# Performance work log

Hardware: AMD Instinct MI355X
Metric: run time of the kernel (lower is better)

The kernel has to match this reference:

```python
import jax, jax.numpy as jnp
import numpy as np

N_NODES = 100000
N_EDGES = 1600000
IN_FEATS = 128
N_HIDDEN = 128
OUT_DIM = 32
BN_EPS = 1e-5


def setup_inputs() -> dict:
    key = jax.random.key(0)
    ks = jax.random.split(key, 12)
    s = 0.05  # weight init scale
    return {
        "features": jax.random.normal(ks[0], (N_NODES, IN_FEATS), dtype=jnp.float32),
        "src": jax.random.randint(ks[1], (N_EDGES,), 0, N_NODES),
        "dst": jax.random.randint(ks[2], (N_EDGES,), 0, N_NODES),
        # layer 0: in_feats -> n_hidden
        "Ws0": jax.random.normal(ks[3], (IN_FEATS, N_HIDDEN), dtype=jnp.float32) * s,
        "Wn0": jax.random.normal(ks[4], (IN_FEATS, N_HIDDEN), dtype=jnp.float32) * s,
        "b0": jnp.zeros((N_HIDDEN,), jnp.float32),
        # layer 1: n_hidden -> n_hidden
        "Ws1": jax.random.normal(ks[5], (N_HIDDEN, N_HIDDEN), dtype=jnp.float32) * s,
        "Wn1": jax.random.normal(ks[6], (N_HIDDEN, N_HIDDEN), dtype=jnp.float32) * s,
        "b1": jnp.zeros((N_HIDDEN,), jnp.float32),
        # layer 2 (output): n_hidden -> out_dim, no activation
        "Ws2": jax.random.normal(ks[7], (N_HIDDEN, OUT_DIM), dtype=jnp.float32) * s,
        "Wn2": jax.random.normal(ks[8], (N_HIDDEN, OUT_DIM), dtype=jnp.float32) * s,
        "b2": jnp.zeros((OUT_DIM,), jnp.float32),
        # batch norms after layers 0 and 1
        "g0": jnp.ones((N_HIDDEN,), jnp.float32),
        "be0": jnp.zeros((N_HIDDEN,), jnp.float32),
        "g1": jnp.ones((N_HIDDEN,), jnp.float32),
        "be1": jnp.zeros((N_HIDDEN,), jnp.float32),
    }


def _sage_mean(h, src, dst, inv_deg, Ws, Wn, b):
    # DGL SAGEConv('mean'): fc_self(h) + fc_neigh(mean of in-neighbor feats)
    agg = jax.ops.segment_sum(h[src], dst, num_segments=N_NODES) * inv_deg
    return h @ Ws + agg @ Wn + b


def _batch_norm(h, gamma, beta):
    mu = jnp.mean(h, axis=0)
    var = jnp.var(h, axis=0)
    return (h - mu) * jax.lax.rsqrt(var + BN_EPS) * gamma + beta


def reference(features, src, dst, Ws0, Wn0, b0, Ws1, Wn1, b1, Ws2, Wn2, b2, g0, be0, g1, be1):
    ones = jnp.ones((N_EDGES,), jnp.float32)
    deg = jax.ops.segment_sum(ones, dst, num_segments=N_NODES)
    inv_deg = (1.0 / jnp.maximum(deg, 1.0))[:, None]  # [N,1]

    # layer 0: SAGEConv internal activation, then BN + external activation
    h = jax.nn.relu(_sage_mean(features, src, dst, inv_deg, Ws0, Wn0, b0))
    h = jax.nn.relu(_batch_norm(h, g0, be0))
    # layer 1 (hidden)
    h = jax.nn.relu(_sage_mean(h, src, dst, inv_deg, Ws1, Wn1, b1))
    h = jax.nn.relu(_batch_norm(h, g1, be1))
    # layer 2 (output): no activation, no BN (idx > n_hidden_layers)
    h = _sage_mean(h, src, dst, inv_deg, Ws2, Wn2, b2)

    # dgl.mean_nodes over a single graph -> [1, out_dim], then softmax over classes
    hg = jnp.mean(h, axis=0, keepdims=True)
    return jax.nn.softmax(hg, axis=1)
```

## Files before the change

kernel.cpp:

```cpp
#include <hip/hip_runtime.h>
#include <hip/hip_bf16.h>

typedef __hip_bfloat16 bf16;
typedef __hip_bfloat162 bf162;

#define NN 100000
#define NE 1600000
#define BN_EPS 1e-5f

#define BSH 8
#define NBUCK ((NN + 255) >> BSH)
#define ABLK 128
#define EPBA ((NE + ABLK - 1) / ABLK)
#define CAP 6144
#define CAPP 5120

struct alignas(16) bf16x8 { bf16 v[8]; };

typedef __bf16 bfrag __attribute__((ext_vector_type(8)));
typedef float f4 __attribute__((ext_vector_type(4)));
typedef float f16v __attribute__((ext_vector_type(16)));
typedef float f2 __attribute__((ext_vector_type(2)));

static __device__ __forceinline__ float b2f(bf16 x){ return __bfloat162float(x); }
static __device__ __forceinline__ bf16 f2b(float x){ return __float2bfloat16(x); }

static __device__ __forceinline__ uint2 pk8_fp8(float x0,float x1,float x2,float x3,
                                                float x4,float x5,float x6,float x7)
{
    int lo = __builtin_amdgcn_cvt_pk_fp8_f32(x0, x1, 0, 0);
    lo = __builtin_amdgcn_cvt_pk_fp8_f32(x2, x3, lo, 1);
    int hi = __builtin_amdgcn_cvt_pk_fp8_f32(x4, x5, 0, 0);
    hi = __builtin_amdgcn_cvt_pk_fp8_f32(x6, x7, hi, 1);
    return make_uint2((unsigned)lo, (unsigned)hi);
}

__global__ __launch_bounds__(256) void k_convert(const float* __restrict__ in,
                                                 unsigned char* __restrict__ outf8, int n)
{
    int i = (blockIdx.x * 256 + threadIdx.x) * 8;
    if (i + 7 < n) {
        float4 a = *(const float4*)(in + i);
        float4 b = *(const float4*)(in + i + 4);
        *(uint2*)(outf8 + i) = pk8_fp8(a.x,a.y,a.z,a.w,b.x,b.y,b.z,b.w);
    }
}

__global__ __launch_bounds__(256) void k_wtrans(const float* __restrict__ W0, const float* __restrict__ W1,
                                                const float* __restrict__ W2, const float* __restrict__ W3,
                                                bf16* __restrict__ T0, bf16* __restrict__ T1,
                                                bf16* __restrict__ T2, bf16* __restrict__ T3)
{
    int m = blockIdx.x >> 6;
    int t = (blockIdx.x & 63) * 256 + threadIdx.x;
    const float* W = (m == 0) ? W0 : (m == 1) ? W1 : (m == 2) ? W2 : W3;
    bf16* T = (m == 0) ? T0 : (m == 1) ? T1 : (m == 2) ? T2 : T3;
    int j = t & 7;
    int lane = (t >> 3) & 63;
    int frag = t >> 9;
    int ks = frag >> 2, ct = frag & 3;
    int k = ks * 16 + (lane >> 5) * 8 + j;
    int n = ct * 32 + (lane & 31);
    T[t] = f2b(W[k * 128 + n]);
}

__global__ __launch_bounds__(256) void k_pa12(const int* __restrict__ src, const int* __restrict__ dst,
                                              int* __restrict__ gcurD, int* __restrict__ gcurS,
                                              unsigned* __restrict__ packD, unsigned* __restrict__ packS)
{
    __shared__ int histD[NBUCK], histS[NBUCK];
    __shared__ int baseD[NBUCK], baseS[NBUCK];
    __shared__ int curD[NBUCK],  curS[NBUCK];
    int t = threadIdx.x;
    for (int i = t; i < NBUCK; i += 256) { histD[i] = 0; histS[i] = 0; curD[i] = 0; curS[i] = 0; }
    __syncthreads();
    int e0 = blockIdx.x * EPBA, e1 = min(e0 + EPBA, NE);
    for (int e = e0 + t; e < e1; e += 256) {
        unsigned bd = ((unsigned)dst[e]) >> BSH;
        unsigned bs = ((unsigned)src[e]) >> BSH;
        if (bd < (unsigned)NBUCK) atomicAdd(&histD[bd], 1);
        if (bs < (unsigned)NBUCK) atomicAdd(&histS[bs], 1);
    }
    __syncthreads();
    for (int i = t; i < NBUCK; i += 256) {
        baseD[i] = (histD[i] > 0) ? atomicAdd(&gcurD[i], histD[i]) : 0;
        baseS[i] = (histS[i] > 0) ? atomicAdd(&gcurS[i], histS[i]) : 0;
    }
    __syncthreads();
    for (int e = e0 + t; e < e1; e += 256) {
        int s = src[e], d = dst[e];
        unsigned bd = ((unsigned)d) >> BSH;
        if (bd < (unsigned)NBUCK) {
            int r = baseD[bd] + atomicAdd(&curD[bd], 1);
            if (r < CAPP)
                packD[(size_t)bd * CAPP + r] = (((unsigned)d & 255u) << 24) | ((unsigned)s & 0xFFFFFFu);
        }
        unsigned bs = ((unsigned)s) >> BSH;
        if (bs < (unsigned)NBUCK) {
            int r = baseS[bs] + atomicAdd(&curS[bs], 1);
            if (r < CAPP)
                packS[(size_t)bs * CAPP + r] = (((unsigned)s & 255u) << 24) | ((unsigned)d & 0xFFFFFFu);
        }
    }
}

__global__ __launch_bounds__(512) void k_bscan(const int* __restrict__ cnt, int* __restrict__ start)
{
    __shared__ int sd[512];
    int t = threadIdx.x;
    int v = (t < NBUCK) ? cnt[t] : 0;
    sd[t] = v;
    __syncthreads();
    for (int o = 1; o < 512; o <<= 1) {
        int x = (t >= o) ? sd[t - o] : 0;
        __syncthreads();
        sd[t] += x;
        __syncthreads();
    }
    if (t < NBUCK) start[t] = sd[t] - v;
    if (t == 0) start[NBUCK] = NE;
}

__global__ __launch_bounds__(256) void k_pbD(const unsigned* __restrict__ packD, const int* __restrict__ bucketStartD,
                                             int* __restrict__ offs, float* __restrict__ invd,
                                             int* __restrict__ esrc)
{
    __shared__ int dcnt[256];
    __shared__ int sscan[256];
    __shared__ int cur[256];
    __shared__ int S[CAP];
    int t = threadIdx.x;
    int b = blockIdx.x;
    int base = b << BSH;
    dcnt[t] = 0;
    cur[t] = 0;
    for (int i = t; i < CAP; i += 256) S[i] = 0;
    __syncthreads();
    int p0 = bucketStartD[b], p1 = bucketStartD[b + 1];
    int cnt = p1 - p0;
    size_t q0 = (size_t)b * CAPP;
    for (int i = t; i < cnt; i += 256)
        atomicAdd(&dcnt[packD[q0 + i] >> 24], 1);
    __syncthreads();
    int my = dcnt[t];
    sscan[t] = my;
    __syncthreads();
    for (int o = 1; o < 256; o <<= 1) {
        int v = (t >= o) ? sscan[t - o] : 0;
        __syncthreads();
        sscan[t] += v;
        __syncthreads();
    }
    int lo = sscan[t] - my;
    if (base + t < NN) {
        offs[base + t] = p0 + lo;
        invd[base + t] = 1.0f / (float)max(my, 1);
    }
    if (b == NBUCK - 1 && t == 0) offs[NN] = NE;
    __syncthreads();
    sscan[t] = lo;
    __syncthreads();
    if (cnt <= CAP) {
        for (int i = t; i < cnt; i += 256) {
            unsigned v = packD[q0 + i];
            unsigned li = v >> 24;
            int pos = sscan[li] + atomicAdd(&cur[li], 1);
            if ((unsigned)pos >= (unsigned)cnt) pos = cnt - 1;
            S[pos] = (int)(v & 0xFFFFFFu);
        }
        __syncthreads();
        for (int i = t; i < cnt; i += 256) esrc[p0 + i] = S[i];
    } else {
        for (int i = t; i < cnt; i += 256) {
            unsigned v = packD[q0 + i];
            unsigned li = v >> 24;
            int pos = sscan[li] + atomicAdd(&cur[li], 1);
            if ((unsigned)pos >= (unsigned)cnt) pos = cnt - 1;
            esrc[p0 + pos] = (int)(v & 0xFFFFFFu);
        }
    }
}

__global__ __launch_bounds__(256) void k_wsrc2(const unsigned* __restrict__ packS, const int* __restrict__ gcurS,
                                               const float* __restrict__ invd, float* __restrict__ wsrc)
{
    __shared__ float wacc[256];
    int t = threadIdx.x;
    wacc[t] = 0.f;
    __syncthreads();
    int b = blockIdx.x;
    int base = b << BSH;
    int cnt = gcurS[b];
    size_t q0 = (size_t)b * CAPP;
    for (int i = t; i < cnt; i += 256) {
        unsigned v = packS[q0 + i];
        unsigned li = v >> 24;
        unsigned dy = v & 0xFFFFFFu;
        if (dy >= (unsigned)NN) dy = 0u;
        atomicAdd(&wacc[li], invd[dy]);
    }
    __syncthreads();
    if (base + t < NN) wsrc[base + t] = wacc[t];
}

__global__ __launch_bounds__(256) void k_aggregate(const unsigned char* __restrict__ inf8, bf16* __restrict__ out,
                                                   const int* __restrict__ offs, const int* __restrict__ esrc,
                                                   const float* __restrict__ invd,
                                                   const float* __restrict__ scsh, int use_ss)
{
    int row = blockIdx.x * 4 + (threadIdx.x >> 6);
    if (row >= NN) return;
    int lane = threadIdx.x & 63;
    int grp = lane >> 4;
    int c0 = (lane & 15) * 8;
    float sc[8], sh[8];
    if (use_ss) {
#pragma unroll
        for (int j = 0; j < 8; j++) { sc[j] = scsh[c0 + j]; sh[j] = scsh[128 + c0 + j]; }
    }
    int e0 = offs[row], e1 = offs[row + 1];
    float a[8];
#pragma unroll
    for (int j = 0; j < 8; j++) a[j] = 0.f;

    auto unpack = [&](uint2 u, float* v) {
        f2 p0 = __builtin_amdgcn_cvt_pk_f32_fp8(u.x, 0);
        f2 p1 = __builtin_amdgcn_cvt_pk_f32_fp8(u.x, 1);
        f2 p2 = __builtin_amdgcn_cvt_pk_f32_fp8(u.y, 0);
        f2 p3 = __builtin_amdgcn_cvt_pk_f32_fp8(u.y, 1);
        v[0]=p0.x; v[1]=p0.y; v[2]=p1.x; v[3]=p1.y; v[4]=p2.x; v[5]=p2.y; v[6]=p3.x; v[7]=p3.y;
    };

    int e = e0 + grp;
    for (; e + 12 < e1; e += 16) {
        int s0 = esrc[e], s1 = esrc[e + 4], s2 = esrc[e + 8], s3 = esrc[e + 12];
        uint2 u0 = *(const uint2*)&inf8[(size_t)s0 * 128 + c0];
        uint2 u1 = *(const uint2*)&inf8[(size_t)s1 * 128 + c0];
        uint2 u2 = *(const uint2*)&inf8[(size_t)s2 * 128 + c0];
        uint2 u3 = *(const uint2*)&inf8[(size_t)s3 * 128 + c0];
        float v0[8], v1[8], v2[8], v3[8];
        unpack(u0, v0); unpack(u1, v1); unpack(u2, v2); unpack(u3, v3);
        if (use_ss) {
#pragma unroll
            for (int j = 0; j < 8; j++)
                a[j] += fmaxf(v0[j] * sc[j] + sh[j], 0.f) + fmaxf(v1[j] * sc[j] + sh[j], 0.f)
                      + fmaxf(v2[j] * sc[j] + sh[j], 0.f) + fmaxf(v3[j] * sc[j] + sh[j], 0.f);
        } else {
#pragma unroll
            for (int j = 0; j < 8; j++)
                a[j] += (v0[j] + v1[j]) + (v2[j] + v3[j]);
        }
    }
    if (e < e1) {
        int i1 = e + 4, i2 = e + 8;
        float m1 = (i1 < e1) ? 1.f : 0.f;
        float m2 = (i2 < e1) ? 1.f : 0.f;
        if (i1 >= e1) i1 = e;
        if (i2 >= e1) i2 = e;
        int s0 = esrc[e], s1 = esrc[i1], s2 = esrc[i2];
        uint2 u0 = *(const uint2*)&inf8[(size_t)s0 * 128 + c0];
        uint2 u1 = *(const uint2*)&inf8[(size_t)s1 * 128 + c0];
        uint2 u2 = *(const uint2*)&inf8[(size_t)s2 * 128 + c0];
        float v0[8], v1[8], v2[8];
        unpack(u0, v0); unpack(u1, v1); unpack(u2, v2);
        if (use_ss) {
#pragma unroll
            for (int j = 0; j < 8; j++)
                a[j] += fmaxf(v0[j] * sc[j] + sh[j], 0.f)
                      + m1 * fmaxf(v1[j] * sc[j] + sh[j], 0.f)
                      + m2 * fmaxf(v2[j] * sc[j] + sh[j], 0.f);
        } else {
#pragma unroll
            for (int j = 0; j < 8; j++)
                a[j] += v0[j] + m1 * v1[j] + m2 * v2[j];
        }
    }
#pragma unroll
    for (int j = 0; j < 8; j++) {
        a[j] += __shfl_xor(a[j], 16);
        a[j] += __shfl_xor(a[j], 32);
    }
    if (grp == 0) {
        float id = invd[row];
        bf16x8 o;
#pragma unroll
        for (int j = 0; j < 8; j++) o.v[j] = f2b(a[j] * id);
        *(bf16x8*)&out[(size_t)row * 128 + c0] = o;
    }
}

#define GM 128
__global__ __launch_bounds__(256, 4) void k_gemm_mfma(const void* __restrict__ HsSrc, int hs_fp8,
                                                      const bf16* __restrict__ Ag,
                                                      const bf16* __restrict__ Wst, const bf16* __restrict__ Wnt,
                                                      const float* __restrict__ bias,
                                                      const float* __restrict__ scsh, int use_ss,
                                                      bf16* __restrict__ outp, unsigned char* __restrict__ outf8,
                                                      float* __restrict__ bnsums)
{
    __shared__ bf16 sout[128][136];
    __shared__ float sredsum[128], sredsq[128];
    int t = threadIdx.x;
    int lane = t & 63;
    int l31 = lane & 31;
    int half = lane >> 5;
    int m0 = (t >> 6) * 32;
    int row0 = blockIdx.x * GM;

    if (t < 128) { sredsum[t] = 0.f; sredsq[t] = 0.f; }
    __syncthreads();

    int arow = row0 + m0 + l31;
    int gc = (arow < NN) ? arow : 0;

    f16v acc[4];
#pragma unroll
    for (int ct = 0; ct < 4; ct++)
#pragma unroll
        for (int r = 0; r < 16; r++) acc[ct][r] = 0.f;

#pragma unroll
    for (int ks = 0; ks < 8; ks++) {
        int k0 = ks * 16 + half * 8;

        bfrag aa = *(const bfrag*)&Ag[(size_t)gc * 128 + k0];
        bfrag ah;
        {
            float hv[8];
            if (hs_fp8) {
                uint2 u = *(const uint2*)((const unsigned char*)HsSrc + (size_t)gc * 128 + k0);
                f2 q0 = __builtin_amdgcn_cvt_pk_f32_fp8(u.x, 0);
                f2 q1 = __builtin_amdgcn_cvt_pk_f32_fp8(u.x, 1);
                f2 q2 = __builtin_amdgcn_cvt_pk_f32_fp8(u.y, 0);
                f2 q3 = __builtin_amdgcn_cvt_pk_f32_fp8(u.y, 1);
                hv[0]=q0.x; hv[1]=q0.y; hv[2]=q1.x; hv[3]=q1.y;
                hv[4]=q2.x; hv[5]=q2.y; hv[6]=q3.x; hv[7]=q3.y;
            } else {
                const float* fp = (const float*)HsSrc + (size_t)gc * 128 + k0;
                float4 x = *(const float4*)fp;
                float4 y = *(const float4*)(fp + 4);
                hv[0]=x.x; hv[1]=x.y; hv[2]=x.z; hv[3]=x.w;
                hv[4]=y.x; hv[5]=y.y; hv[6]=y.z; hv[7]=y.w;
            }
            if (use_ss) {
                float4 s0 = *(const float4*)&scsh[k0];
                float4 s1 = *(const float4*)&scsh[k0 + 4];
                float4 h0 = *(const float4*)&scsh[128 + k0];
                float4 h1 = *(const float4*)&scsh[128 + k0 + 4];
                hv[0] = fmaxf(hv[0]*s0.x + h0.x, 0.f); hv[1] = fmaxf(hv[1]*s0.y + h0.y, 0.f);
                hv[2] = fmaxf(hv[2]*s0.z + h0.z, 0.f); hv[3] = fmaxf(hv[3]*s0.w + h0.w, 0.f);
                hv[4] = fmaxf(hv[4]*s1.x + h1.x, 0.f); hv[5] = fmaxf(hv[5]*s1.y + h1.y, 0.f);
                hv[6] = fmaxf(hv[6]*s1.z + h1.z, 0.f); hv[7] = fmaxf(hv[7]*s1.w + h1.w, 0.f);
            }
#pragma unroll
            for (int j = 0; j < 8; j++) ah[j] = (__bf16)hv[j];
        }

#pragma unroll
        for (int ct = 0; ct < 4; ct++) {
            size_t fo = (size_t)((ks * 4 + ct) * 64 + lane) * 8;
            bfrag bs  = *(const bfrag*)&Wst[fo];
            bfrag bnf = *(const bfrag*)&Wnt[fo];
            acc[ct] = __builtin_amdgcn_mfma_f32_32x32x16_bf16(ah, bs,  acc[ct], 0, 0, 0);
            acc[ct] = __builtin_amdgcn_mfma_f32_32x32x16_bf16(aa, bnf, acc[ct], 0, 0, 0);
        }
    }

    float psum[4], psq[4];
#pragma unroll
    for (int ct = 0; ct < 4; ct++) {
        int col = ct * 32 + l31;
        float bv = bias[col];
        float s = 0.f, s2 = 0.f;
#pragma unroll
        for (int r = 0; r < 16; r++) {
            int lrow = m0 + 4 * half + (r & 3) + 8 * (r >> 2);
            float v = fmaxf(acc[ct][r] + bv, 0.f);
            sout[lrow][col] = f2b(v);
            if (row0 + lrow < NN) { s += v; s2 += v * v; }
        }
        psum[ct] = s; psq[ct] = s2;
    }
#pragma unroll
    for (int ct = 0; ct < 4; ct++) {
        psum[ct] += __shfl_xor(psum[ct], 32);
        psq[ct]  += __shfl_xor(psq[ct], 32);
    }
    if (lane < 32) {
#pragma unroll
        for (int ct = 0; ct < 4; ct++) {
            atomicAdd(&sredsum[ct * 32 + lane], psum[ct]);
            atomicAdd(&sredsq[ct * 32 + lane],  psq[ct]);
        }
    }

#pragma unroll
    for (int i = 0; i < 8; i++) {
        int idx = i * 64 + lane;
        int row = m0 + (idx >> 4);
        int c16 = idx & 15;
        int grow = row0 + row;
        if (grow < NN) {
            bf16x8 ov = *(const bf16x8*)&sout[row][c16 * 8];
            if (outp) *(bf16x8*)&outp[(size_t)grow * 128 + c16 * 8] = ov;
            if (outf8) {
                *(uint2*)&outf8[(size_t)grow * 128 + c16 * 8] =
                    pk8_fp8(b2f(ov.v[0]), b2f(ov.v[1]), b2f(ov.v[2]), b2f(ov.v[3]),
                            b2f(ov.v[4]), b2f(ov.v[5]), b2f(ov.v[6]), b2f(ov.v[7]));
            }
        }
    }

    __syncthreads();
    if (t < 128) {
        atomicAdd(&bnsums[t], sredsum[t]);
        atomicAdd(&bnsums[128 + t], sredsq[t]);
    }
}

__global__ void k_bn_fin(const float* __restrict__ sums, const float* __restrict__ g,
                         const float* __restrict__ be, float* __restrict__ scsh)
{
    int t = threadIdx.x;
    if (t < 128) {
        float mu = sums[t] / (float)NN;
        float var = sums[128 + t] / (float)NN - mu * mu;
        float sc = g[t] * rsqrtf(var + BN_EPS);
        scsh[t] = sc;
        scsh[128 + t] = be[t] - mu * sc;
    }
}

__global__ __launch_bounds__(256) void k_l2_reduce(const bf16* __restrict__ h, const float* __restrict__ scsh,
                                                   const float* __restrict__ wsrc, float* __restrict__ ue)
{
    __shared__ float su[128], se[128];
    int t = threadIdx.x;
    if (t < 128) { su[t] = 0.f; se[t] = 0.f; }
    __syncthreads();
    int c0 = (t & 15) * 8;
    int rof = t >> 4;
    float sc[8], sh[8];
#pragma unroll
    for (int j = 0; j < 8; j++) { sc[j] = scsh[c0 + j]; sh[j] = scsh[128 + c0 + j]; }
    float u[8], es[8];
#pragma unroll
    for (int j = 0; j < 8; j++) { u[j] = 0.f; es[j] = 0.f; }
    int rpb = (NN + gridDim.x - 1) / gridDim.x;
    int r0 = blockIdx.x * rpb;
    int r1 = min(r0 + rpb, NN);
    for (int r = r0 + rof; r < r1; r += 16) {
        bf16x8 v = *(const bf16x8*)&h[(size_t)r * 128 + c0];
        float w = wsrc[r];
#pragma unroll
        for (int j = 0; j < 8; j++) {
            float x = fmaxf(b2f(v.v[j]) * sc[j] + sh[j], 0.f);
            u[j] += x; es[j] += w * x;
        }
    }
#pragma unroll
    for (int j = 0; j < 8; j++) { atomicAdd(&su[c0 + j], u[j]); atomicAdd(&se[c0 + j], es[j]); }
    __syncthreads();
    if (t < 128) { atomicAdd(&ue[t], su[t]); atomicAdd(&ue[128 + t], se[t]); }
}

__global__ void k_final(const float* __restrict__ ue, const float* __restrict__ Ws2,
                        const float* __restrict__ Wn2, const float* __restrict__ b2,
                        float* __restrict__ out)
{
    __shared__ float logit[32];
    int t = threadIdx.x;
    const float inv = 1.0f / (float)NN;
    if (t < 32) {
        float acc = b2[t];
        for (int k = 0; k < 128; k++)
            acc += (ue[k] * inv) * Ws2[k * 32 + t] + (ue[128 + k] * inv) * Wn2[k * 32 + t];
        logit[t] = acc;
    }
    __syncthreads();
    if (t < 32) {
        float m = -1e30f;
        for (int j = 0; j < 32; j++) m = fmaxf(m, logit[j]);
        float s = 0.f;
        for (int j = 0; j < 32; j++) s += expf(logit[j] - m);
        out[t] = expf(logit[t] - m) / s;
    }
}

extern "C" void kernel_launch(void* const* d_in, const int* in_sizes, int n_in,
                              void* d_out, int out_size, void* d_ws, size_t ws_size,
                              hipStream_t stream)
{
    const float* feat = (const float*)d_in[0];
    const int*   src  = (const int*)d_in[1];
    const int*   dst  = (const int*)d_in[2];
    const float* Ws0  = (const float*)d_in[3];
    const float* Wn0  = (const float*)d_in[4];
    const float* b0   = (const float*)d_in[5];
    const float* Ws1  = (const float*)d_in[6];
    const float* Wn1  = (const float*)d_in[7];
    const float* b1   = (const float*)d_in[8];
    const float* Ws2  = (const float*)d_in[9];
    const float* Wn2  = (const float*)d_in[10];
    const float* b2   = (const float*)d_in[11];
    const float* g0   = (const float*)d_in[12];
    const float* be0  = (const float*)d_in[13];
    const float* g1   = (const float*)d_in[14];
    const float* be1  = (const float*)d_in[15];

    char* p = (char*)d_ws;
    auto alloc = [&](size_t b) -> void* {
        void* r = (void*)p;
        p += (b + 255) & ~(size_t)255;
        return r;
    };
    bf16* A      = (bf16*)alloc((size_t)NN * 128 * 2);
    unsigned char* F8 = (unsigned char*)alloc((size_t)NN * 128);
    unsigned* packS = (unsigned*)alloc((size_t)NBUCK * CAPP * 4);
    int*  esrc   = (int*)alloc((size_t)NE * 4);
    int*  offs   = (int*)alloc((size_t)(NN + 1) * 4);
    float* invd  = (float*)alloc((size_t)NN * 4);
    float* wsrc  = (float*)alloc((size_t)NN * 4);
    char* zstart = p;
    int*  gcurD  = (int*)alloc((NBUCK + 1) * 4);
    int*  gcurS  = (int*)alloc((NBUCK + 1) * 4);
    float* bn0   = (float*)alloc(256 * 4);
    float* bn1   = (float*)alloc(256 * 4);
    float* ue    = (float*)alloc(256 * 4);
    size_t zlen = (size_t)(p - zstart);
    float* scsh0 = (float*)alloc(256 * 4);
    float* scsh1 = (float*)alloc(256 * 4);
    bf16* Ws0t   = (bf16*)alloc(16384 * 2);
    bf16* Wn0t   = (bf16*)alloc(16384 * 2);
    bf16* Ws1t   = (bf16*)alloc(16384 * 2);
    bf16* Wn1t   = (bf16*)alloc(16384 * 2);
    int*  bucketStartD = (int*)alloc((NBUCK + 1) * 4);

    unsigned* packD = (unsigned*)A;

    hipMemsetAsync(zstart, 0, zlen, stream);

    const int GB = (NN + GM - 1) / GM;

    k_convert<<<(NN * 128) / (256 * 8), 256, 0, stream>>>(feat, F8, NN * 128);
    k_wtrans<<<256, 256, 0, stream>>>(Ws0, Wn0, Ws1, Wn1, Ws0t, Wn0t, Ws1t, Wn1t);

    k_pa12<<<ABLK, 256, 0, stream>>>(src, dst, gcurD, gcurS, packD, packS);
    k_bscan<<<1, 512, 0, stream>>>(gcurD, bucketStartD);
    k_pbD<<<NBUCK, 256, 0, stream>>>(packD, bucketStartD, offs, invd, esrc);
    k_wsrc2<<<NBUCK, 256, 0, stream>>>(packS, gcurS, invd, wsrc);

    k_aggregate<<<(NN + 3) / 4, 256, 0, stream>>>(F8, A, offs, esrc, invd, nullptr, 0);
    k_gemm_mfma<<<GB, 256, 0, stream>>>(feat, 0, A, Ws0t, Wn0t, b0, nullptr, 0, nullptr, F8, bn0);
    k_bn_fin<<<1, 128, 0, stream>>>(bn0, g0, be0, scsh0);

    k_aggregate<<<(NN + 3) / 4, 256, 0, stream>>>(F8, A, offs, esrc, invd, scsh0, 1);
    k_gemm_mfma<<<GB, 256, 0, stream>>>(F8, 1, A, Ws1t, Wn1t, b1, scsh0, 1, A, nullptr, bn1);
    k_bn_fin<<<1, 128, 0, stream>>>(bn1, g1, be1, scsh1);

    k_l2_reduce<<<256, 256, 0, stream>>>(A, scsh1, wsrc, ue);
    k_final<<<1, 64, 0, stream>>>(ue, Ws2, Wn2, b2, (float*)d_out);
}
```

Before: 436.6 us.

## Split aggregate gather columns into four block slices with 16-way edge parallelism

The neighbor-aggregation kernel now launches four times as many blocks, and each block handles one 32-column slice of four rows. A wavefront spreads each row's edges across 16 lane groups of 4 lanes each, instead of 4 groups of 16 lanes with a 4-way unrolled loop and a masked tail. The aim is more edges in flight per wavefront and a simpler loop without the tail code. In exchange, each edge gathers only 32 bytes per slice, every row's edge list is read four times, and the cross-lane reduction needs two extra shuffle steps.

```diff
diff --git a/kernel.cpp b/kernel.cpp
--- a/kernel.cpp
+++ b/kernel.cpp
@@ -208,11 +208,12 @@
                                                    const float* __restrict__ invd,
                                                    const float* __restrict__ scsh, int use_ss)
 {
-    int row = blockIdx.x * 4 + (threadIdx.x >> 6);
+    int slice = blockIdx.x & 3;
+    int row = (blockIdx.x >> 2) * 4 + (threadIdx.x >> 6);
     if (row >= NN) return;
     int lane = threadIdx.x & 63;
-    int grp = lane >> 4;
-    int c0 = (lane & 15) * 8;
+    int grp = lane >> 2;
+    int c0 = slice * 32 + (lane & 3) * 8;
     float sc[8], sh[8];
     if (use_ss) {
 #pragma unroll
@@ -223,60 +224,26 @@
 #pragma unroll
     for (int j = 0; j < 8; j++) a[j] = 0.f;
 
-    auto unpack = [&](uint2 u, float* v) {
+    for (int e = e0 + grp; e < e1; e += 16) {
+        int s = esrc[e];
+        uint2 u = *(const uint2*)&inf8[(size_t)s * 128 + c0];
         f2 p0 = __builtin_amdgcn_cvt_pk_f32_fp8(u.x, 0);
         f2 p1 = __builtin_amdgcn_cvt_pk_f32_fp8(u.x, 1);
         f2 p2 = __builtin_amdgcn_cvt_pk_f32_fp8(u.y, 0);
         f2 p3 = __builtin_amdgcn_cvt_pk_f32_fp8(u.y, 1);
-        v[0]=p0.x; v[1]=p0.y; v[2]=p1.x; v[3]=p1.y; v[4]=p2.x; v[5]=p2.y; v[6]=p3.x; v[7]=p3.y;
-    };
-
-    int e = e0 + grp;
-    for (; e + 12 < e1; e += 16) {
-        int s0 = esrc[e], s1 = esrc[e + 4], s2 = esrc[e + 8], s3 = esrc[e + 12];
-        uint2 u0 = *(const uint2*)&inf8[(size_t)s0 * 128 + c0];
-        uint2 u1 = *(const uint2*)&inf8[(size_t)s1 * 128 + c0];
-        uint2 u2 = *(const uint2*)&inf8[(size_t)s2 * 128 + c0];
-        uint2 u3 = *(const uint2*)&inf8[(size_t)s3 * 128 + c0];
-        float v0[8], v1[8], v2[8], v3[8];
-        unpack(u0, v0); unpack(u1, v1); unpack(u2, v2); unpack(u3, v3);
+        float v[8] = {p0.x,p0.y,p1.x,p1.y,p2.x,p2.y,p3.x,p3.y};
         if (use_ss) {
 #pragma unroll
-            for (int j = 0; j < 8; j++)
-                a[j] += fmaxf(v0[j] * sc[j] + sh[j], 0.f) + fmaxf(v1[j] * sc[j] + sh[j], 0.f)
-                      + fmaxf(v2[j] * sc[j] + sh[j], 0.f) + fmaxf(v3[j] * sc[j] + sh[j], 0.f);
+            for (int j = 0; j < 8; j++) a[j] += fmaxf(v[j] * sc[j] + sh[j], 0.f);
         } else {
 #pragma unroll
-            for (int j = 0; j < 8; j++)
-                a[j] += (v0[j] + v1[j]) + (v2[j] + v3[j]);
-        }
-    }
-    if (e < e1) {
-        int i1 = e + 4, i2 = e + 8;
-        float m1 = (i1 < e1) ? 1.f : 0.f;
-        float m2 = (i2 < e1) ? 1.f : 0.f;
-        if (i1 >= e1) i1 = e;
-        if (i2 >= e1) i2 = e;
-        int s0 = esrc[e], s1 = esrc[i1], s2 = esrc[i2];
-        uint2 u0 = *(const uint2*)&inf8[(size_t)s0 * 128 + c0];
-        uint2 u1 = *(const uint2*)&inf8[(size_t)s1 * 128 + c0];
-        uint2 u2 = *(const uint2*)&inf8[(size_t)s2 * 128 + c0];
-        float v0[8], v1[8], v2[8];
-        unpack(u0, v0); unpack(u1, v1); unpack(u2, v2);
-        if (use_ss) {
-#pragma unroll
-            for (int j = 0; j < 8; j++)
-                a[j] += fmaxf(v0[j] * sc[j] + sh[j], 0.f)
-                      + m1 * fmaxf(v1[j] * sc[j] + sh[j], 0.f)
-                      + m2 * fmaxf(v2[j] * sc[j] + sh[j], 0.f);
-        } else {
-#pragma unroll
-            for (int j = 0; j < 8; j++)
-                a[j] += v0[j] + m1 * v1[j] + m2 * v2[j];
+            for (int j = 0; j < 8; j++) a[j] += v[j];
         }
     }
 #pragma unroll
     for (int j = 0; j < 8; j++) {
+        a[j] += __shfl_xor(a[j], 4);
+        a[j] += __shfl_xor(a[j], 8);
         a[j] += __shfl_xor(a[j], 16);
         a[j] += __shfl_xor(a[j], 32);
     }
@@ -541,6 +508,7 @@
     hipMemsetAsync(zstart, 0, zlen, stream);
 
     const int GB = (NN + GM - 1) / GM;
+    const int AGB = ((NN + 3) / 4) * 4;
 
     k_convert<<<(NN * 128) / (256 * 8), 256, 0, stream>>>(feat, F8, NN * 128);
     k_wtrans<<<256, 256, 0, stream>>>(Ws0, Wn0, Ws1, Wn1, Ws0t, Wn0t, Ws1t, Wn1t);
@@ -550,11 +518,11 @@
     k_pbD<<<NBUCK, 256, 0, stream>>>(packD, bucketStartD, offs, invd, esrc);
     k_wsrc2<<<NBUCK, 256, 0, stream>>>(packS, gcurS, invd, wsrc);
 
-    k_aggregate<<<(NN + 3) / 4, 256, 0, stream>>>(F8, A, offs, esrc, invd, nullptr, 0);
+    k_aggregate<<<AGB, 256, 0, stream>>>(F8, A, offs, esrc, invd, nullptr, 0);
     k_gemm_mfma<<<GB, 256, 0, stream>>>(feat, 0, A, Ws0t, Wn0t, b0, nullptr, 0, nullptr, F8, bn0);
     k_bn_fin<<<1, 128, 0, stream>>>(bn0, g0, be0, scsh0);
 
-    k_aggregate<<<(NN + 3) / 4, 256, 0, stream>>>(F8, A, offs, esrc, invd, scsh0, 1);
+    k_aggregate<<<AGB, 256, 0, stream>>>(F8, A, offs, esrc, invd, scsh0, 1);
     k_gemm_mfma<<<GB, 256, 0, stream>>>(F8, 1, A, Ws1t, Wn1t, b1, scsh0, 1, A, nullptr, bn1);
     k_bn_fin<<<1, 128, 0, stream>>>(bn1, g1, be1, scsh1);
 
```

Result: slower. 623.5 us (+42.8%).
